# Optimization experiments

Hardware: AMD Instinct MI355X
Metric: run time of the kernel (lower is better)

The kernel has to match this reference:

```python
import jax, jax.numpy as jnp
import numpy as np

K = 1024      # num_embeddings
D = 256       # embedding_dim
BETA = 0.25
DECAY = 0.99
EPS = 1e-05


def setup_inputs() -> dict:
    key = jax.random.key(0)
    k1, k2 = jax.random.split(key)
    z_e = jax.random.normal(k1, (32, D, 32, 32), dtype=jnp.float32)
    embedding = jax.random.normal(k2, (K, D), dtype=jnp.float32)
    ema_cluster_size = jnp.zeros((K,), dtype=jnp.float32)
    ema_w = embedding  # buffer initialized as a clone of the codebook
    return {"z_e": z_e, "embedding": embedding,
            "ema_cluster_size": ema_cluster_size, "ema_w": ema_w}


def reference(z_e, embedding, ema_cluster_size, ema_w):
    B, Dd, H, W = z_e.shape
    # (B, D, H, W) -> (N, D)
    flat_z = jnp.transpose(z_e, (0, 2, 3, 1)).reshape(-1, Dd)

    # L2 distance argmin (||z||^2 + ||e||^2 - 2 z.e)
    dist = (jnp.sum(flat_z * flat_z, axis=1, keepdims=True)
            + jnp.sum(embedding * embedding, axis=1)
            - 2.0 * flat_z @ embedding.T)
    indices = jnp.argmin(dist, axis=1)  # (N,)

    # EMA update (operates on detached values; buffers updated in-place in torch)
    flat_z_sg = jax.lax.stop_gradient(flat_z)
    cluster_size = jax.ops.segment_sum(
        jnp.ones_like(indices, dtype=z_e.dtype), indices, num_segments=K)
    new_ema_cluster_size = DECAY * ema_cluster_size + (1.0 - DECAY) * cluster_size
    dw = jax.ops.segment_sum(flat_z_sg, indices, num_segments=K)  # one_hot.T @ flat_z
    new_ema_w = DECAY * ema_w + (1.0 - DECAY) * dw
    new_embedding = new_ema_w / (new_ema_cluster_size + EPS)[:, None]

    # Gather uses the *updated* codebook (torch copies into the buffer first)
    z_q_flat = new_embedding[indices]                      # (N, D)
    z_q = jnp.transpose(z_q_flat.reshape(B, H, W, Dd), (0, 3, 1, 2))

    # Straight-through estimator + commitment loss
    z_q_st = z_e + jax.lax.stop_gradient(z_q - z_e)
    vq_loss = BETA * jnp.mean((z_e - jax.lax.stop_gradient(z_q)) ** 2)

    return (z_q_st, vq_loss, indices.reshape(B, H, W),
            new_embedding, new_ema_cluster_size, new_ema_w)
```

## Files before the change

### kernel.cpp

```cpp
#include <hip/hip_runtime.h>
#include <stdint.h>

#define N_ROWS 32768
#define K_CODES 1024
#define D_DIM 256
#define NELEM 8388608

#define WS_COUNTS 0
#define WS_LOSS 1030
#define WS_ENORM 263168
#define WS_ROWBEST_BYTES 1056768
#define WS_IDX_BYTES 1318912

#define O_ZQ 0
#define O_LOSS 8388608
#define O_IDX 8388609
#define O_EMB 8421377
#define O_CS 8683521
#define O_EMAW 8684545

#define EP_BYTE_OFF 33685520

typedef _Float16 half8 __attribute__((ext_vector_type(8)));
typedef float f32x16 __attribute__((ext_vector_type(16)));

__device__ __forceinline__ unsigned int fenc(float f) {
    unsigned int u = __float_as_uint(f);
    return (u & 0x80000000u) ? ~u : (u | 0x80000000u);
}
__device__ __forceinline__ unsigned long long umin64(unsigned long long a, unsigned long long b) {
    return a < b ? a : b;
}
__device__ __forceinline__ void gll16(const void* g, void* l) {
    __builtin_amdgcn_global_load_lds((const __attribute__((address_space(1))) void*)g,
                                     (__attribute__((address_space(3))) void*)l, 16, 0, 0);
}

__global__ __launch_bounds__(256) void k_conv_e(const float* __restrict__ emb,
                                                _Float16* __restrict__ Ep,
                                                float* __restrict__ enorm,
                                                float* __restrict__ ws) {
    int k = blockIdx.x, d = threadIdx.x;
    int gid = k * 256 + d;
    if (gid < 2048) ws[gid] = 0.0f;
    unsigned long long* rb = (unsigned long long*)((char*)ws + WS_ROWBEST_BYTES);
    if (gid < N_ROWS) rb[gid] = 0xFFFFFFFFFFFFFFFFull;

    float v = emb[k * 256 + d];
    _Float16 h = (_Float16)v;
    _Float16 l = (_Float16)(v - (float)h);
    int s = d >> 3, sub = d & 7;
    Ep[((size_t)s * 1024 + k) * 8 + sub] = h;
    Ep[((size_t)(32 + s) * 1024 + k) * 8 + sub] = l;
    float sq = v * v;
    #pragma unroll
    for (int off = 32; off >= 1; off >>= 1) sq += __shfl_down(sq, off, 64);
    __shared__ float red[4];
    if ((d & 63) == 0) red[d >> 6] = sq;
    __syncthreads();
    if (d == 0) enorm[k] = (red[0] + red[1]) + (red[2] + red[3]);
}

__global__ __launch_bounds__(256) void k_conv_z(const float* __restrict__ z_e,
                                                _Float16* __restrict__ Zp,
                                                float* __restrict__ lossacc) {
    __shared__ float lt[64 * 68];
    __shared__ float red[4];
    int t = threadIdx.x;
    int hw0 = blockIdx.x * 64, d0 = blockIdx.y * 64, b = blockIdx.z;
    const float* src = z_e + (size_t)b * 262144 + (size_t)d0 * 1024 + hw0;
    int dl = t >> 4, hl = (t & 15) * 4;
    float sq = 0.0f;
    #pragma unroll
    for (int i = 0; i < 4; i++) {
        int d = dl + i * 16;
        float4 v = *(const float4*)(src + (size_t)d * 1024 + hl);
        sq += v.x * v.x + v.y * v.y + v.z * v.z + v.w * v.w;
        lt[(hl + 0) * 68 + d] = v.x;
        lt[(hl + 1) * 68 + d] = v.y;
        lt[(hl + 2) * 68 + d] = v.z;
        lt[(hl + 3) * 68 + d] = v.w;
    }
    __syncthreads();
    int hr = t >> 2, seg = t & 3;
    int n = b * 1024 + hw0 + hr;
    int sg0 = (d0 >> 3) + seg * 2;
    half8 hi[2], lo[2];
    #pragma unroll
    for (int p = 0; p < 2; p++) {
        #pragma unroll
        for (int j = 0; j < 8; j++) {
            float v = lt[hr * 68 + seg * 16 + p * 8 + j];
            _Float16 h = (_Float16)v;
            hi[p][j] = h;
            lo[p][j] = (_Float16)(v - (float)h);
        }
    }
    *(half8*)(Zp + ((size_t)(sg0 + 0) * 32768 + n) * 8) = hi[0];
    *(half8*)(Zp + ((size_t)(sg0 + 1) * 32768 + n) * 8) = hi[1];
    *(half8*)(Zp + ((size_t)(32 + sg0) * 32768 + n) * 8) = lo[0];
    *(half8*)(Zp + ((size_t)(33 + sg0) * 32768 + n) * 8) = lo[1];
    #pragma unroll
    for (int off = 32; off >= 1; off >>= 1) sq += __shfl_down(sq, off, 64);
    if ((t & 63) == 0) red[t >> 6] = sq;
    __syncthreads();
    if (t == 0) atomicAdd(lossacc, (red[0] + red[1]) + (red[2] + red[3]));
}

__global__ __launch_bounds__(512) void k_mm(const _Float16* __restrict__ Zp,
                                            const _Float16* __restrict__ Ep,
                                            const float* __restrict__ enorm,
                                            unsigned long long* __restrict__ row_best) {
    __shared__ __align__(16) char smem[131072];

    int t = threadIdx.x;
    int lane = t & 63, wv = t >> 6;
    int b = blockIdx.x;
    int wgid = (b & 7) * 64 + (b >> 3);
    int rt = wgid >> 2;
    int ct = wgid & 3;
    int row0 = rt * 256, code0 = ct * 256;

    int wr = wv >> 2, wc = wv & 3;
    int m31 = lane & 31, ko = lane >> 5;

    f32x16 acc[4][2];
    #pragma unroll
    for (int m = 0; m < 4; m++)
        #pragma unroll
        for (int n = 0; n < 2; n++)
            #pragma unroll
            for (int r = 0; r < 16; r++) acc[m][n][r] = 0.0f;

    const char* zbase = (const char*)Zp + ((size_t)wv * 32768 + row0 + lane) * 16;
    const char* ebase = (const char*)Ep + ((size_t)wv * 1024 + code0 + lane) * 16;
    _Float16* zlds = (_Float16*)smem + wv * 256 * 8;
    _Float16* elds = (_Float16*)(smem + 32768) + wv * 256 * 8;

    auto STAGE = [&](int c, int buf) {
        int kz = (c < 8) ? c : (c - 8);
        int ge = (c < 4) ? c * 8 : (c < 8) ? (c - 4) * 8 : 32 + (c - 8) * 8;
        const char* zg = zbase + (size_t)kz * 8 * 32768 * 16;
        const char* eg = ebase + (size_t)ge * 1024 * 16;
        _Float16* zl = zlds + buf * 32768;
        _Float16* el = elds + buf * 32768;
        #pragma unroll
        for (int i = 0; i < 4; i++) {
            gll16(zg + (size_t)i * 64 * 16, zl + i * 512);
            gll16(eg + (size_t)i * 64 * 16, el + i * 512);
        }
    };

    STAGE(0, 0);
    STAGE(1, 1);
    asm volatile("s_waitcnt vmcnt(8)" ::: "memory");
    __builtin_amdgcn_s_barrier();
    asm volatile("" ::: "memory");

    for (int c = 0; c < 12; c++) {
        const _Float16* Za = (const _Float16*)(smem + (c & 1) * 65536);
        const _Float16* Ea = (const _Float16*)(smem + (c & 1) * 65536 + 32768);
        __builtin_amdgcn_s_setprio(1);
        #pragma unroll
        for (int ks = 0; ks < 4; ks++) {
            int sseg = 2 * ks + ko;
            half8 a0 = *(const half8*)(Za + (sseg * 256 + wr * 128 +  0 + m31) * 8);
            half8 a1 = *(const half8*)(Za + (sseg * 256 + wr * 128 + 32 + m31) * 8);
            half8 a2 = *(const half8*)(Za + (sseg * 256 + wr * 128 + 64 + m31) * 8);
            half8 a3 = *(const half8*)(Za + (sseg * 256 + wr * 128 + 96 + m31) * 8);
            half8 b0 = *(const half8*)(Ea + (sseg * 256 + wc * 64 +  0 + m31) * 8);
            half8 b1 = *(const half8*)(Ea + (sseg * 256 + wc * 64 + 32 + m31) * 8);
            acc[0][0] = __builtin_amdgcn_mfma_f32_32x32x16_f16(a0, b0, acc[0][0], 0, 0, 0);
            acc[0][1] = __builtin_amdgcn_mfma_f32_32x32x16_f16(a0, b1, acc[0][1], 0, 0, 0);
            acc[1][0] = __builtin_amdgcn_mfma_f32_32x32x16_f16(a1, b0, acc[1][0], 0, 0, 0);
            acc[1][1] = __builtin_amdgcn_mfma_f32_32x32x16_f16(a1, b1, acc[1][1], 0, 0, 0);
            acc[2][0] = __builtin_amdgcn_mfma_f32_32x32x16_f16(a2, b0, acc[2][0], 0, 0, 0);
            acc[2][1] = __builtin_amdgcn_mfma_f32_32x32x16_f16(a2, b1, acc[2][1], 0, 0, 0);
            acc[3][0] = __builtin_amdgcn_mfma_f32_32x32x16_f16(a3, b0, acc[3][0], 0, 0, 0);
            acc[3][1] = __builtin_amdgcn_mfma_f32_32x32x16_f16(a3, b1, acc[3][1], 0, 0, 0);
        }
        __builtin_amdgcn_s_setprio(0);
        asm volatile("s_waitcnt lgkmcnt(0)" ::: "memory");
        __builtin_amdgcn_s_barrier();
        if (c < 10) STAGE(c + 2, c & 1);
        if (c < 11) {
            if (c < 10) asm volatile("s_waitcnt vmcnt(8)" ::: "memory");
            else        asm volatile("s_waitcnt vmcnt(0)" ::: "memory");
            __builtin_amdgcn_s_barrier();
            asm volatile("" ::: "memory");
        }
    }

    unsigned long long* slot = (unsigned long long*)smem;
    float en0 = enorm[code0 + wc * 64 + m31];
    float en1 = enorm[code0 + wc * 64 + 32 + m31];
    unsigned int col0 = code0 + wc * 64 + m31;
    unsigned int col1 = col0 + 32;

    if (wc == 0) {
        #pragma unroll
        for (int m = 0; m < 4; m++)
            #pragma unroll
            for (int j = 0; j < 16; j++) {
                int row = wr * 128 + m * 32 + 4 * ko + (j & 3) + 8 * (j >> 2);
                unsigned long long p0 = ((unsigned long long)fenc(en0 - 2.0f * acc[m][0][j]) << 32) | col0;
                unsigned long long p1 = ((unsigned long long)fenc(en1 - 2.0f * acc[m][1][j]) << 32) | col1;
                slot[row * 32 + ((m31 + row) & 31)] = umin64(p0, p1);
            }
    }
    __syncthreads();
    if (wc != 0) {
        #pragma unroll
        for (int m = 0; m < 4; m++)
            #pragma unroll
            for (int j = 0; j < 16; j++) {
                int row = wr * 128 + m * 32 + 4 * ko + (j & 3) + 8 * (j >> 2);
                unsigned long long p0 = ((unsigned long long)fenc(en0 - 2.0f * acc[m][0][j]) << 32) | col0;
                unsigned long long p1 = ((unsigned long long)fenc(en1 - 2.0f * acc[m][1][j]) << 32) | col1;
                atomicMin(&slot[row * 32 + ((m31 + row) & 31)], umin64(p0, p1));
            }
    }
    __syncthreads();
    if (t < 256) {
        unsigned long long mm = slot[t * 32 + (t & 31)];
        #pragma unroll
        for (int i = 1; i < 32; i++) mm = umin64(mm, slot[t * 32 + ((i + t) & 31)]);
        atomicMin(&row_best[row0 + t], mm);
    }
}

__global__ __launch_bounds__(256) void k_fin_idx(const unsigned long long* __restrict__ rb,
                                                 int* __restrict__ idxs,
                                                 float* __restrict__ counts,
                                                 float* __restrict__ out) {
    __shared__ float hist[K_CODES];
    int t = threadIdx.x;
    #pragma unroll
    for (int j = 0; j < 4; j++) hist[j * 256 + t] = 0.0f;
    __syncthreads();
    int i = blockIdx.x * 256 + t;
    int id = (int)(rb[i] & 0xFFFFFFFFull);
    idxs[i] = id;
    out[O_IDX + i] = (float)id;
    atomicAdd(&hist[id], 1.0f);
    __syncthreads();
    #pragma unroll
    for (int j = 0; j < 4; j++) {
        float h = hist[j * 256 + t];
        if (h != 0.0f) atomicAdd(&counts[j * 256 + t], h);
    }
}

__global__ __launch_bounds__(512) void k_dw(const float* __restrict__ z_e,
                                            const int* __restrict__ idxs,
                                            float* __restrict__ dw) {
    __shared__ float acc[K_CODES];
    int t = threadIdx.x;
    int d = blockIdx.x;
    #pragma unroll
    for (int j = 0; j < 2; j++) acc[j * 512 + t] = 0.0f;
    __syncthreads();
    for (int b = 0; b < 32; b++) {
        int2 id2 = *(const int2*)(idxs + b * 1024 + t * 2);
        float2 v = *(const float2*)(z_e + (size_t)b * 262144 + (size_t)d * 1024 + t * 2);
        atomicAdd(&acc[id2.x], v.x);
        atomicAdd(&acc[id2.y], v.y);
    }
    __syncthreads();
    float* pr = dw + (size_t)d * 1024;
    #pragma unroll
    for (int j = 0; j < 2; j++) pr[j * 512 + t] = acc[j * 512 + t];
}

__global__ __launch_bounds__(256) void k_red(const float* __restrict__ dw,
                                             const float* __restrict__ ema_cs,
                                             const float* __restrict__ ema_w,
                                             const float* __restrict__ counts,
                                             float* __restrict__ lossacc,
                                             float* __restrict__ out) {
    __shared__ float tile[64 * 69];
    __shared__ float csl[64];
    __shared__ float craw[64];
    __shared__ float red[4];
    int t = threadIdx.x;
    int k0 = blockIdx.x * 64, d0 = blockIdx.y * 64;
    int dr = t >> 4, kc = t & 15;
    if (t < 64) {
        float c = counts[k0 + t];
        craw[t] = c;
        csl[t] = 0.99f * ema_cs[k0 + t] + 0.01f * c;
    }
    #pragma unroll
    for (int q = 0; q < 4; q++) {
        float4 v = *(const float4*)(dw + (size_t)(d0 + dr + 16 * q) * 1024 + k0 + kc * 4);
        float* p = tile + (dr + 16 * q) * 69 + kc * 4;
        p[0] = v.x; p[1] = v.y; p[2] = v.z; p[3] = v.w;
    }
    __syncthreads();
    int kk = t >> 2, dq = t & 3;
    int k = k0 + kk;
    float inv = 1.0f / (csl[kk] + 1e-5f);
    float cr = craw[kk];
    float lterm = 0.0f;
    #pragma unroll
    for (int j4 = 0; j4 < 4; j4++) {
        int dd = dq * 16 + j4 * 4;
        size_t kd = (size_t)k * 256 + d0 + dd;
        float4 w = *(const float4*)(ema_w + kd);
        float s0 = tile[(dd + 0) * 69 + kk];
        float s1 = tile[(dd + 1) * 69 + kk];
        float s2 = tile[(dd + 2) * 69 + kk];
        float s3 = tile[(dd + 3) * 69 + kk];
        float4 nw;
        nw.x = 0.99f * w.x + 0.01f * s0;
        nw.y = 0.99f * w.y + 0.01f * s1;
        nw.z = 0.99f * w.z + 0.01f * s2;
        nw.w = 0.99f * w.w + 0.01f * s3;
        *(float4*)(out + O_EMAW + kd) = nw;
        float4 ne = {nw.x * inv, nw.y * inv, nw.z * inv, nw.w * inv};
        *(float4*)(out + O_EMB + kd) = ne;
        lterm += ne.x * (cr * ne.x - 2.0f * s0);
        lterm += ne.y * (cr * ne.y - 2.0f * s1);
        lterm += ne.z * (cr * ne.z - 2.0f * s2);
        lterm += ne.w * (cr * ne.w - 2.0f * s3);
    }
    if (blockIdx.y == 0 && t < 64) out[O_CS + k0 + t] = csl[t];
    #pragma unroll
    for (int off = 32; off >= 1; off >>= 1) lterm += __shfl_down(lterm, off, 64);
    if ((t & 63) == 0) red[t >> 6] = lterm;
    __syncthreads();
    if (t == 0) atomicAdd(lossacc, (red[0] + red[1]) + (red[2] + red[3]));
}

__global__ __launch_bounds__(256) void k_bcast(const int* __restrict__ idxs,
                                               const float* __restrict__ lossacc,
                                               float* __restrict__ out) {
    __shared__ float lt[64 * 68];
    __shared__ int sid[64];
    int t = threadIdx.x;
    int hw0 = blockIdx.x * 64, d0 = blockIdx.y * 64, b = blockIdx.z;
    if (t < 64) sid[t] = idxs[b * 1024 + hw0 + t];
    __syncthreads();
    int r = t >> 2, c = t & 3;
    const float* nrow = out + O_EMB + (size_t)sid[r] * 256 + d0;
    #pragma unroll
    for (int it = 0; it < 4; it++) {
        int dd = it * 16 + c * 4;
        float4 q = *(const float4*)(nrow + dd);
        float* p = lt + r * 68 + dd;
        p[0] = q.x; p[1] = q.y; p[2] = q.z; p[3] = q.w;
    }
    __syncthreads();
    int dl = t >> 4, hl = (t & 15) * 4;
    float* dst = out + O_ZQ + (size_t)b * 262144 + (size_t)d0 * 1024 + hw0;
    #pragma unroll
    for (int i = 0; i < 4; i++) {
        int d = dl + i * 16;
        float4 w;
        w.x = lt[(hl + 0) * 68 + d];
        w.y = lt[(hl + 1) * 68 + d];
        w.z = lt[(hl + 2) * 68 + d];
        w.w = lt[(hl + 3) * 68 + d];
        *(float4*)(dst + (size_t)d * 1024 + hl) = w;
    }
    if (blockIdx.x == 0 && blockIdx.y == 0 && blockIdx.z == 0 && t == 0)
        out[O_LOSS] = lossacc[0] * 2.9802322387695312e-08f;
}

extern "C" void kernel_launch(void* const* d_in, const int* in_sizes, int n_in,
                              void* d_out, int out_size, void* d_ws, size_t ws_size,
                              hipStream_t stream) {
    const float* z_e = (const float*)d_in[0];
    const float* emb = (const float*)d_in[1];
    const float* ema_cs = (const float*)d_in[2];
    const float* ema_w = (const float*)d_in[3];
    float* out = (float*)d_out;
    float* ws = (float*)d_ws;

    float* counts = ws + WS_COUNTS;
    float* lossacc = ws + WS_LOSS;
    float* enorm = ws + WS_ENORM;
    unsigned long long* row_best = (unsigned long long*)((char*)d_ws + WS_ROWBEST_BYTES);
    int* idxs = (int*)((char*)d_ws + WS_IDX_BYTES);

    _Float16* Zp = (_Float16*)d_out;
    _Float16* Ep = (_Float16*)((char*)d_out + EP_BYTE_OFF);
    float* dw = (float*)d_out;

    k_conv_e<<<1024, 256, 0, stream>>>(emb, Ep, enorm, ws);
    k_conv_z<<<dim3(16, 4, 32), 256, 0, stream>>>(z_e, Zp, lossacc);
    k_mm<<<512, 512, 0, stream>>>(Zp, Ep, enorm, row_best);
    k_fin_idx<<<128, 256, 0, stream>>>(row_best, idxs, counts, out);
    k_dw<<<256, 512, 0, stream>>>(z_e, idxs, dw);
    k_red<<<dim3(16, 4), 256, 0, stream>>>(dw, ema_cs, ema_w, counts, lossacc, out);
    k_bcast<<<dim3(16, 4, 32), 256, 0, stream>>>(idxs, lossacc, out);
}
```

Baseline: 236.0 us.

## Halve k_mm LDS stage size and fold index finalisation into k_dw

The GEMM kernel now stages half as much K-depth per step (24 steps of 2 k-slices instead of 12 of 4), cutting shared memory from 128KB to 64KB, which may allow more concurrent blocks per CU or lower LDS pressure. Separately, the k_fin_idx launch is removed: k_dw and k_bcast read indices directly from the packed row_best values, and k_dw also writes the float indices and builds the per-code histogram. This saves one kernel launch and one intermediate index buffer, at the cost of more barriers per GEMM and reading 8-byte entries instead of 4-byte ones.

New measurement: 240.9 us. 1.02x slower.

```diff
diff --git a/kernel.cpp b/kernel.cpp
--- a/kernel.cpp
+++ b/kernel.cpp
@@ -10,7 +10,6 @@
 #define WS_LOSS 1030
 #define WS_ENORM 263168
 #define WS_ROWBEST_BYTES 1056768
-#define WS_IDX_BYTES 1318912
 
 #define O_ZQ 0
 #define O_LOSS 8388608
@@ -111,7 +110,7 @@
                                             const _Float16* __restrict__ Ep,
                                             const float* __restrict__ enorm,
                                             unsigned long long* __restrict__ row_best) {
-    __shared__ __align__(16) char smem[131072];
+    __shared__ __align__(16) char smem[65536];
 
     int t = threadIdx.x;
     int lane = t & 63, wv = t >> 6;
@@ -132,37 +131,38 @@
             #pragma unroll
             for (int r = 0; r < 16; r++) acc[m][n][r] = 0.0f;
 
-    const char* zbase = (const char*)Zp + ((size_t)wv * 32768 + row0 + lane) * 16;
-    const char* ebase = (const char*)Ep + ((size_t)wv * 1024 + code0 + lane) * 16;
-    _Float16* zlds = (_Float16*)smem + wv * 256 * 8;
-    _Float16* elds = (_Float16*)(smem + 32768) + wv * 256 * 8;
+    int sseg_st = wv >> 1;
+    int rowbase = (wv & 1) * 128;
+    const char* zgw = (const char*)Zp + ((size_t)row0 + rowbase + lane) * 16;
+    const char* egw = (const char*)Ep + ((size_t)code0 + rowbase + lane) * 16;
+
+    auto zsb = [](int tt) { return (tt < 16 ? tt : tt - 16) * 4; };
+    auto esb = [](int tt) { return tt < 8 ? tt * 4 : (tt < 16 ? (tt - 8) * 4 : 32 + (tt - 16) * 4); };
 
     auto STAGE = [&](int c, int buf) {
-        int kz = (c < 8) ? c : (c - 8);
-        int ge = (c < 4) ? c * 8 : (c < 8) ? (c - 4) * 8 : 32 + (c - 8) * 8;
-        const char* zg = zbase + (size_t)kz * 8 * 32768 * 16;
-        const char* eg = ebase + (size_t)ge * 1024 * 16;
-        _Float16* zl = zlds + buf * 32768;
-        _Float16* el = elds + buf * 32768;
-        #pragma unroll
-        for (int i = 0; i < 4; i++) {
-            gll16(zg + (size_t)i * 64 * 16, zl + i * 512);
-            gll16(eg + (size_t)i * 64 * 16, el + i * 512);
-        }
+        int zs = zsb(c) + sseg_st, es = esb(c) + sseg_st;
+        const char* zg = zgw + (size_t)zs * 32768 * 16;
+        const char* eg = egw + (size_t)es * 1024 * 16;
+        char* zl = smem + buf * 32768 + sseg_st * 4096 + rowbase * 16;
+        char* el = smem + buf * 32768 + 16384 + sseg_st * 4096 + rowbase * 16;
+        gll16(zg, zl);
+        gll16(zg + 64 * 16, zl + 64 * 16);
+        gll16(eg, el);
+        gll16(eg + 64 * 16, el + 64 * 16);
     };
 
     STAGE(0, 0);
     STAGE(1, 1);
-    asm volatile("s_waitcnt vmcnt(8)" ::: "memory");
+    asm volatile("s_waitcnt vmcnt(4)" ::: "memory");
     __builtin_amdgcn_s_barrier();
     asm volatile("" ::: "memory");
 
-    for (int c = 0; c < 12; c++) {
-        const _Float16* Za = (const _Float16*)(smem + (c & 1) * 65536);
-        const _Float16* Ea = (const _Float16*)(smem + (c & 1) * 65536 + 32768);
+    for (int c = 0; c < 24; c++) {
+        const _Float16* Za = (const _Float16*)(smem + (c & 1) * 32768);
+        const _Float16* Ea = (const _Float16*)(smem + (c & 1) * 32768 + 16384);
         __builtin_amdgcn_s_setprio(1);
         #pragma unroll
-        for (int ks = 0; ks < 4; ks++) {
+        for (int ks = 0; ks < 2; ks++) {
             int sseg = 2 * ks + ko;
             half8 a0 = *(const half8*)(Za + (sseg * 256 + wr * 128 +  0 + m31) * 8);
             half8 a1 = *(const half8*)(Za + (sseg * 256 + wr * 128 + 32 + m31) * 8);
@@ -182,9 +182,9 @@
         __builtin_amdgcn_s_setprio(0);
         asm volatile("s_waitcnt lgkmcnt(0)" ::: "memory");
         __builtin_amdgcn_s_barrier();
-        if (c < 10) STAGE(c + 2, c & 1);
-        if (c < 11) {
-            if (c < 10) asm volatile("s_waitcnt vmcnt(8)" ::: "memory");
+        if (c < 22) STAGE(c + 2, c & 1);
+        if (c < 23) {
+            if (c < 22) asm volatile("s_waitcnt vmcnt(4)" ::: "memory");
             else        asm volatile("s_waitcnt vmcnt(0)" ::: "memory");
             __builtin_amdgcn_s_barrier();
             asm volatile("" ::: "memory");
@@ -229,31 +229,11 @@
     }
 }
 
-__global__ __launch_bounds__(256) void k_fin_idx(const unsigned long long* __restrict__ rb,
-                                                 int* __restrict__ idxs,
-                                                 float* __restrict__ counts,
-                                                 float* __restrict__ out) {
-    __shared__ float hist[K_CODES];
-    int t = threadIdx.x;
-    #pragma unroll
-    for (int j = 0; j < 4; j++) hist[j * 256 + t] = 0.0f;
-    __syncthreads();
-    int i = blockIdx.x * 256 + t;
-    int id = (int)(rb[i] & 0xFFFFFFFFull);
-    idxs[i] = id;
-    out[O_IDX + i] = (float)id;
-    atomicAdd(&hist[id], 1.0f);
-    __syncthreads();
-    #pragma unroll
-    for (int j = 0; j < 4; j++) {
-        float h = hist[j * 256 + t];
-        if (h != 0.0f) atomicAdd(&counts[j * 256 + t], h);
-    }
-}
-
 __global__ __launch_bounds__(512) void k_dw(const float* __restrict__ z_e,
-                                            const int* __restrict__ idxs,
-                                            float* __restrict__ dw) {
+                                            const unsigned long long* __restrict__ rb,
+                                            float* __restrict__ counts,
+                                            float* __restrict__ dw,
+                                            float* __restrict__ out) {
     __shared__ float acc[K_CODES];
     int t = threadIdx.x;
     int d = blockIdx.x;
@@ -261,15 +241,31 @@
     for (int j = 0; j < 2; j++) acc[j * 512 + t] = 0.0f;
     __syncthreads();
     for (int b = 0; b < 32; b++) {
-        int2 id2 = *(const int2*)(idxs + b * 1024 + t * 2);
+        ulonglong2 rr = *(const ulonglong2*)(rb + (size_t)b * 1024 + t * 2);
         float2 v = *(const float2*)(z_e + (size_t)b * 262144 + (size_t)d * 1024 + t * 2);
-        atomicAdd(&acc[id2.x], v.x);
-        atomicAdd(&acc[id2.y], v.y);
+        atomicAdd(&acc[(int)(rr.x & 0xFFFFFFFFull)], v.x);
+        atomicAdd(&acc[(int)(rr.y & 0xFFFFFFFFull)], v.y);
     }
     __syncthreads();
     float* pr = dw + (size_t)d * 1024;
     #pragma unroll
     for (int j = 0; j < 2; j++) pr[j * 512 + t] = acc[j * 512 + t];
+    __syncthreads();
+    #pragma unroll
+    for (int j = 0; j < 2; j++) acc[j * 512 + t] = 0.0f;
+    __syncthreads();
+    if (t < 128) {
+        int i = d * 128 + t;
+        int id = (int)(rb[i] & 0xFFFFFFFFull);
+        out[O_IDX + i] = (float)id;
+        atomicAdd(&acc[id], 1.0f);
+    }
+    __syncthreads();
+    #pragma unroll
+    for (int j = 0; j < 2; j++) {
+        float h = acc[j * 512 + t];
+        if (h != 0.0f) atomicAdd(&counts[j * 512 + t], h);
+    }
 }
 
 __global__ __launch_bounds__(256) void k_red(const float* __restrict__ dw,
@@ -332,14 +328,14 @@
     if (t == 0) atomicAdd(lossacc, (red[0] + red[1]) + (red[2] + red[3]));
 }
 
-__global__ __launch_bounds__(256) void k_bcast(const int* __restrict__ idxs,
+__global__ __launch_bounds__(256) void k_bcast(const unsigned long long* __restrict__ rb,
                                                const float* __restrict__ lossacc,
                                                float* __restrict__ out) {
     __shared__ float lt[64 * 68];
     __shared__ int sid[64];
     int t = threadIdx.x;
     int hw0 = blockIdx.x * 64, d0 = blockIdx.y * 64, b = blockIdx.z;
-    if (t < 64) sid[t] = idxs[b * 1024 + hw0 + t];
+    if (t < 64) sid[t] = (int)(rb[b * 1024 + hw0 + t] & 0xFFFFFFFFull);
     __syncthreads();
     int r = t >> 2, c = t & 3;
     const float* nrow = out + O_EMB + (size_t)sid[r] * 256 + d0;
@@ -381,7 +377,6 @@
     float* lossacc = ws + WS_LOSS;
     float* enorm = ws + WS_ENORM;
     unsigned long long* row_best = (unsigned long long*)((char*)d_ws + WS_ROWBEST_BYTES);
-    int* idxs = (int*)((char*)d_ws + WS_IDX_BYTES);
 
     _Float16* Zp = (_Float16*)d_out;
     _Float16* Ep = (_Float16*)((char*)d_out + EP_BYTE_OFF);
@@ -390,8 +385,7 @@
     k_conv_e<<<1024, 256, 0, stream>>>(emb, Ep, enorm, ws);
     k_conv_z<<<dim3(16, 4, 32), 256, 0, stream>>>(z_e, Zp, lossacc);
     k_mm<<<512, 512, 0, stream>>>(Zp, Ep, enorm, row_best);
-    k_fin_idx<<<128, 256, 0, stream>>>(row_best, idxs, counts, out);
-    k_dw<<<256, 512, 0, stream>>>(z_e, idxs, dw);
+    k_dw<<<256, 512, 0, stream>>>(z_e, row_best, counts, dw, out);
     k_red<<<dim3(16, 4), 256, 0, stream>>>(dw, ema_cs, ema_w, counts, lossacc, out);
-    k_bcast<<<dim3(16, 4, 32), 256, 0, stream>>>(idxs, lossacc, out);
-}
+    k_bcast<<<dim3(16, 4, 32), 256, 0, stream>>>(row_best, lossacc, out);
+}
```
